# Performance work log

Hardware: AMD Instinct MI355X
Metric: run time of the kernel (lower is better)

Reference implementation:

```python
import jax, jax.numpy as jnp
import numpy as np

LRELU = 0.2


def _gru(x, Wi, Wh, bi, bh):
    # x: [B,T,D]; Wi: [3H,D]; Wh: [3H,H]; PyTorch GRU equations.
    B, T, D = x.shape
    H = Wh.shape[1]
    xW = jnp.einsum('btd,gd->btg', x, Wi) + bi  # precompute input projections
    def step(h, xw):
        gh = h @ Wh.T + bh
        xr, xz, xn = jnp.split(xw, 3, axis=-1)
        hr, hz, hn = jnp.split(gh, 3, axis=-1)
        r = jax.nn.sigmoid(xr + hr)
        z = jax.nn.sigmoid(xz + hz)
        n = jnp.tanh(xn + r * hn)
        h_new = (1.0 - z) * n + z * h
        return h_new, h_new
    h0 = jnp.zeros((B, H), x.dtype)
    hT, hs = jax.lax.scan(step, h0, jnp.swapaxes(xW, 0, 1))
    return jnp.swapaxes(hs, 0, 1), hT


def _gatv2(x, W, b, a, bias):
    # x: [B,N,F]; W: [2F,E]; lin([v_i||v_j]) == x_i@W1 + x_j@W2 + b (avoids materializing concat)
    F = x.shape[-1]
    W1, W2 = W[:F], W[F:]
    g1 = x @ W1            # [B,N,E]
    g2 = x @ W2 + b        # [B,N,E]
    z = jax.nn.leaky_relu(g1[:, :, None, :] + g2[:, None, :, :], LRELU)  # [B,N,N,E]
    e = jnp.einsum('bije,e->bij', z, a) + bias
    att = jax.nn.softmax(e, axis=2)
    return jax.nn.sigmoid(jnp.einsum('bij,bjf->bif', att, x))


def setup_inputs() -> dict:
    B, W, K, H, KS = 16, 256, 64, 150, 7
    key = jax.random.key(0)
    ks = jax.random.split(key, 32)
    def rn(i, sh, scale):
        return jax.random.normal(ks[i], sh, jnp.float32) * scale
    inp = {}
    inp['x'] = jax.random.normal(ks[0], (B, W, K), jnp.float32)
    inp['conv_w'] = rn(1, (K, K, KS), 1.0 / np.sqrt(K * KS))
    inp['conv_b'] = rn(2, (K,), 0.02)
    inp['fW'] = rn(3, (2 * W, 2 * W), 1.0 / np.sqrt(2 * W))
    inp['fb'] = rn(4, (2 * W,), 0.02)
    inp['fa'] = rn(5, (2 * W,), 1.0 / np.sqrt(2 * W))
    inp['fbias'] = rn(6, (K, K), 0.02)
    inp['tW'] = rn(7, (2 * K, 2 * K), 1.0 / np.sqrt(2 * K))
    inp['tb'] = rn(8, (2 * K,), 0.02)
    inp['ta'] = rn(9, (2 * K,), 1.0 / np.sqrt(2 * K))
    inp['tbias'] = rn(10, (W, W), 0.02)
    inp['gWi'] = rn(11, (3 * H, 3 * K), 1.0 / np.sqrt(H))
    inp['gWh'] = rn(12, (3 * H, H), 1.0 / np.sqrt(H))
    inp['gbi'] = rn(13, (3 * H,), 0.02)
    inp['gbh'] = rn(14, (3 * H,), 0.02)
    inp['f0w'] = rn(15, (H, H), 1.0 / np.sqrt(H))
    inp['f0b'] = rn(16, (H,), 0.02)
    inp['f1w'] = rn(17, (H, K), 1.0 / np.sqrt(H))
    inp['f1b'] = rn(18, (K,), 0.02)
    inp['rWi'] = rn(19, (3 * H, H), 1.0 / np.sqrt(H))
    inp['rWh'] = rn(20, (3 * H, H), 1.0 / np.sqrt(H))
    inp['rbi'] = rn(21, (3 * H,), 0.02)
    inp['rbh'] = rn(22, (3 * H,), 0.02)
    inp['rfw'] = rn(23, (H, K), 1.0 / np.sqrt(H))
    inp['rfb'] = rn(24, (K,), 0.02)
    return inp


def reference(x, conv_w, conv_b, fW, fb, fa, fbias, tW, tb, ta, tbias,
              gWi, gWh, gbi, gbh, f0w, f0b, f1w, f1b,
              rWi, rWh, rbi, rbh, rfw, rfb):
    B, Wsz, K = x.shape
    pad = (conv_w.shape[2] - 1) // 2
    # ConvLayer: permute -> constant pad -> conv1d -> relu -> permute back
    x_ncw = jnp.swapaxes(x, 1, 2)  # [B,K,W]
    x_pad = jnp.pad(x_ncw, ((0, 0), (0, 0), (pad, pad)))
    xc = jax.lax.conv_general_dilated(x_pad, conv_w, (1,), 'VALID',
                                      dimension_numbers=('NCW', 'OIW', 'NCW'))
    xc = jax.nn.relu(xc + conv_b[None, :, None])
    xc = jnp.swapaxes(xc, 1, 2)  # [B,W,K]
    # Feature GAT over nodes (K), temporal GAT over time (W)
    h_feat = jnp.swapaxes(_gatv2(jnp.swapaxes(xc, 1, 2), fW, fb, fa, fbias), 1, 2)  # [B,W,K]
    h_temp = _gatv2(xc, tW, tb, ta, tbias)  # [B,W,K]
    h_cat = jnp.concatenate([xc, h_feat, h_temp], axis=2)  # [B,W,3K]
    _, h_end = _gru(h_cat, gWi, gWh, gbi, gbh)  # [B,H]
    # Forecasting MLP (n_layers=1 -> two Linear layers)
    predictions = jax.nn.relu(h_end @ f0w + f0b) @ f1w + f1b  # [B,K]
    # Reconstruction: repeat_interleave over dim 1 then view(B, W, -1)
    H = h_end.shape[1]
    h_rep = jnp.repeat(h_end, Wsz, axis=1).reshape(B, Wsz, H)
    dec_out, _ = _gru(h_rep, rWi, rWh, rbi, rbh)  # [B,W,H]
    recons = dec_out @ rfw + rfb  # [B,W,K]
    return predictions, recons
```

## Files before the change

kernel.cpp:

```cpp
#include <hip/hip_runtime.h>
#include <hip/hip_fp16.h>

typedef _Float16 h2f __attribute__((ext_vector_type(2)));

__device__ __forceinline__ float dot2f(unsigned a, unsigned b, float c) {
#if __has_builtin(__builtin_amdgcn_fdot2)
  return __builtin_amdgcn_fdot2(__builtin_bit_cast(h2f, a),
                                __builtin_bit_cast(h2f, b), c, false);
#else
  h2f x = __builtin_bit_cast(h2f, a);
  h2f y = __builtin_bit_cast(h2f, b);
  return c + (float)x[0] * (float)y[0] + (float)x[1] * (float)y[1];
#endif
}

__device__ __forceinline__ float sigf(float x) { return 1.0f / (1.0f + __expf(-x)); }
__device__ __forceinline__ float tanhfast(float x) {
  float e = __expf(-2.0f * fabsf(x));
  float r = (1.0f - e) / (1.0f + e);
  return (x < 0.0f) ? -r : r;
}
__device__ __forceinline__ float lrelu(float x) { return x > 0.0f ? x : 0.2f * x; }

__global__ void k_prep(const float* __restrict__ conv_w, const float* __restrict__ gWi,
                       const float* __restrict__ gWh, const float* __restrict__ rWh,
                       const float* __restrict__ rWi,
                       float* __restrict__ cwT, float* __restrict__ gWiT,
                       unsigned* __restrict__ gWhP, unsigned* __restrict__ rWhP,
                       float* __restrict__ pref) {
  const int N0 = 64 * 64 * 7;
  const int N1 = 192 * 450;
  const int N2 = 36000;
  const int N3 = 36000;
  const int N4 = 450;
  int total = N0 + N1 + N2 + N3 + N4;
  for (int idx = blockIdx.x * blockDim.x + threadIdx.x; idx < total;
       idx += gridDim.x * blockDim.x) {
    if (idx < N0) {
      int k = idx & 63; int is = idx >> 6; int i = is / 7; int s = is - i * 7;
      cwT[idx] = conv_w[(k * 64 + i) * 7 + s];
    } else if (idx < N0 + N1) {
      int j = idx - N0; int g = j % 450; int d = j / 450;
      gWiT[j] = gWi[g * 192 + d];
    } else if (idx < N0 + N1 + N2 + N3) {
      int u = idx - (N0 + N1);
      const float* W = gWh;
      unsigned* dst = gWhP;
      if (u >= N2) { u -= N2; W = rWh; dst = rWhP; }
      int c = u & 3; int q = u >> 2;
      int i = q / 600; int t6 = q - i * 600;
      int i2 = t6 >> 2, qt = t6 & 3;
      int gg = i / 5, li = i - gg * 5;
      int jj = qt * 20 + li * 4 + c;
      int e0 = 2 * jj, e1 = 2 * jj + 1;
      int row = i2 + gg * 150;
      float a = (e0 < 150) ? W[row * 150 + e0] : 0.f;
      float b = (e1 < 150) ? W[row * 150 + e1] : 0.f;
      __half2 h = __floats2half2_rn(a, b);
      dst[u] = *reinterpret_cast<unsigned*>(&h);
    } else {
      int g = idx - (N0 + N1 + N2 + N3);
      float run = 0.f;
      pref[g] = 0.f;
      for (int j = 0; j < 150; ++j) { run += rWi[g * 150 + j]; pref[(j + 1) * 450 + g] = run; }
    }
  }
}

__global__ __launch_bounds__(256) void k_conv(const float* __restrict__ x,
                                              const float* __restrict__ cwT,
                                              const float* __restrict__ conv_b,
                                              float* __restrict__ xc) {
  __shared__ float xs[22 * 64];
  int b = blockIdx.y, t0 = blockIdx.x * 16, tid = threadIdx.x;
  for (int l = tid; l < 22 * 64; l += 256) {
    int r = l >> 6, i = l & 63;
    int t = t0 - 3 + r;
    xs[l] = (t >= 0 && t < 256) ? x[(b * 256 + t) * 64 + i] : 0.f;
  }
  __syncthreads();
  int k = tid & 63, tg = tid >> 6;
  float bias = conv_b[k];
  float acc[4] = {bias, bias, bias, bias};
  for (int i = 0; i < 64; ++i) {
#pragma unroll
    for (int s = 0; s < 7; ++s) {
      float wv = cwT[(i * 7 + s) * 64 + k];
#pragma unroll
      for (int q = 0; q < 4; ++q)
        acc[q] += xs[(tg * 4 + q + s) * 64 + i] * wv;
    }
  }
#pragma unroll
  for (int q = 0; q < 4; ++q)
    xc[(b * 256 + t0 + tg * 4 + q) * 64 + k] = fmaxf(acc[q], 0.f);
}

__global__ __launch_bounds__(512) void k_featg(const float* __restrict__ xc,
                                               const float* __restrict__ fW,
                                               const float* __restrict__ fb,
                                               float* __restrict__ g1f,
                                               float* __restrict__ g2fT) {
  __shared__ float xsL[256 * 8];
  int b = blockIdx.y, i0 = blockIdx.x * 8, e = threadIdx.x;
  for (int l = e; l < 2048; l += 512) {
    int t = l >> 3, ii = l & 7;
    xsL[l] = xc[(b * 256 + t) * 64 + i0 + ii];
  }
  __syncthreads();
  float a1[8] = {}, a2[8] = {};
  for (int t = 0; t < 256; ++t) {
    float w1 = fW[t * 512 + e];
    float w2 = fW[(256 + t) * 512 + e];
#pragma unroll
    for (int ii = 0; ii < 8; ++ii) {
      float s = xsL[t * 8 + ii];
      a1[ii] += s * w1; a2[ii] += s * w2;
    }
  }
  float fbe = fb[e];
#pragma unroll
  for (int ii = 0; ii < 8; ++ii)
    g1f[(b * 64 + i0 + ii) * 512 + e] = a1[ii];
  float4 v0 = make_float4(a2[0] + fbe, a2[1] + fbe, a2[2] + fbe, a2[3] + fbe);
  float4 v1 = make_float4(a2[4] + fbe, a2[5] + fbe, a2[6] + fbe, a2[7] + fbe);
  float4* p = reinterpret_cast<float4*>(&g2fT[(b * 512 + e) * 64 + i0]);
  p[0] = v0; p[1] = v1;
}

__global__ __launch_bounds__(256) void k_feata(const float* __restrict__ xc,
                                               const float* __restrict__ g1f,
                                               const float* __restrict__ g2fT,
                                               const float* __restrict__ fa,
                                               const float* __restrict__ fbias,
                                               float* __restrict__ h_feat) {
  __shared__ float g1L[512], faL[512], part[4 * 64], attL[64];
  int b = blockIdx.y, i = blockIdx.x, tid = threadIdx.x;
  for (int l = tid; l < 512; l += 256) {
    g1L[l] = g1f[(b * 64 + i) * 512 + l];
    faL[l] = fa[l];
  }
  __syncthreads();
  int q = tid >> 6, j = tid & 63;
  float acc = 0.f;
  for (int e = q * 128; e < q * 128 + 128; ++e) {
    float z = g1L[e] + g2fT[(b * 512 + e) * 64 + j];
    acc += faL[e] * lrelu(z);
  }
  part[q * 64 + j] = acc;
  __syncthreads();
  if (tid < 64) {
    float ev = part[tid] + part[64 + tid] + part[128 + tid] + part[192 + tid] +
               fbias[i * 64 + tid];
    float m = ev;
#pragma unroll
    for (int off = 32; off > 0; off >>= 1) m = fmaxf(m, __shfl_xor(m, off));
    float p = __expf(ev - m);
    float s = p;
#pragma unroll
    for (int off = 32; off > 0; off >>= 1) s += __shfl_xor(s, off);
    attL[tid] = p / s;
  }
  __syncthreads();
  float o = 0.f;
  for (int jj = 0; jj < 64; ++jj)
    o += attL[jj] * xc[(b * 256 + tid) * 64 + jj];
  h_feat[(b * 256 + tid) * 64 + i] = sigf(o);
}

__global__ __launch_bounds__(256) void k_tempg(const float* __restrict__ xc,
                                               const float* __restrict__ tW,
                                               const float* __restrict__ tb,
                                               float* __restrict__ g1t,
                                               float* __restrict__ g2tT) {
  __shared__ float xsL[16 * 64];
  int b = blockIdx.y, t0 = blockIdx.x * 16, tid = threadIdx.x;
  int e = tid & 127, th = tid >> 7;
  for (int l = tid; l < 1024; l += 256)
    xsL[l] = xc[(b * 256 + t0) * 64 + l];
  __syncthreads();
  float a1[8] = {}, a2[8] = {};
  for (int k = 0; k < 64; ++k) {
    float w1 = tW[k * 128 + e];
    float w2 = tW[(64 + k) * 128 + e];
#pragma unroll
    for (int tt = 0; tt < 8; ++tt) {
      float s = xsL[(th * 8 + tt) * 64 + k];
      a1[tt] += s * w1; a2[tt] += s * w2;
    }
  }
  float tbe = tb[e];
#pragma unroll
  for (int tt = 0; tt < 8; ++tt)
    g1t[(b * 256 + t0 + th * 8 + tt) * 128 + e] = a1[tt];
  float4 v0 = make_float4(a2[0] + tbe, a2[1] + tbe, a2[2] + tbe, a2[3] + tbe);
  float4 v1 = make_float4(a2[4] + tbe, a2[5] + tbe, a2[6] + tbe, a2[7] + tbe);
  float4* p = reinterpret_cast<float4*>(&g2tT[(b * 128 + e) * 256 + t0 + th * 8]);
  p[0] = v0; p[1] = v1;
}

__global__ __launch_bounds__(256) void k_tempa(const float* __restrict__ xc,
                                               const float* __restrict__ g1t,
                                               const float* __restrict__ g2tT,
                                               const float* __restrict__ ta,
                                               const float* __restrict__ tbias,
                                               float* __restrict__ h_temp) {
  __shared__ float g1L[4 * 128], taL[128], eL[4 * 256];
  int b = blockIdx.y, i0 = blockIdx.x * 4, tid = threadIdx.x;
  for (int l = tid; l < 512; l += 256)
    g1L[l] = g1t[(b * 256 + i0) * 128 + l];
  if (tid < 128) taL[tid] = ta[tid];
  __syncthreads();
  float acc[4] = {};
  for (int e = 0; e < 128; ++e) {
    float g2 = g2tT[(b * 128 + e) * 256 + tid];
    float tae = taL[e];
#pragma unroll
    for (int ii = 0; ii < 4; ++ii)
      acc[ii] += tae * lrelu(g1L[ii * 128 + e] + g2);
  }
#pragma unroll
  for (int ii = 0; ii < 4; ++ii)
    eL[ii * 256 + tid] = acc[ii] + tbias[(i0 + ii) * 256 + tid];
  __syncthreads();
  int wv = tid >> 6, ln = tid & 63;
  {
    float v0 = eL[wv * 256 + ln], v1 = eL[wv * 256 + 64 + ln];
    float v2 = eL[wv * 256 + 128 + ln], v3 = eL[wv * 256 + 192 + ln];
    float m = fmaxf(fmaxf(v0, v1), fmaxf(v2, v3));
#pragma unroll
    for (int off = 32; off > 0; off >>= 1) m = fmaxf(m, __shfl_xor(m, off));
    float p0 = __expf(v0 - m), p1 = __expf(v1 - m);
    float p2 = __expf(v2 - m), p3 = __expf(v3 - m);
    float s = p0 + p1 + p2 + p3;
#pragma unroll
    for (int off = 32; off > 0; off >>= 1) s += __shfl_xor(s, off);
    float rs = 1.f / s;
    eL[wv * 256 + ln] = p0 * rs; eL[wv * 256 + 64 + ln] = p1 * rs;
    eL[wv * 256 + 128 + ln] = p2 * rs; eL[wv * 256 + 192 + ln] = p3 * rs;
  }
  __syncthreads();
  int ii = tid >> 6, k = tid & 63;
  float o = 0.f;
  for (int j = 0; j < 256; ++j)
    o += eL[ii * 256 + j] * xc[(b * 256 + j) * 64 + k];
  h_temp[(b * 256 + i0 + ii) * 64 + k] = sigf(o);
}

__global__ __launch_bounds__(256) void k_xw(const float* __restrict__ xc,
                                            const float* __restrict__ h_feat,
                                            const float* __restrict__ h_temp,
                                            const float* __restrict__ gWiT,
                                            const float* __restrict__ gbi,
                                            float* __restrict__ xW) {
  __shared__ float hc[16 * 192];
  int b = blockIdx.z, t0 = blockIdx.y * 16, g0 = blockIdx.x * 128;
  int tid = threadIdx.x;
  for (int l = tid; l < 16 * 192; l += 256) {
    int tt = l / 192, d = l - tt * 192;
    int row = (b * 256 + t0 + tt) * 64;
    float v;
    if (d < 64) v = xc[row + d];
    else if (d < 128) v = h_feat[row + d - 64];
    else v = h_temp[row + d - 128];
    hc[l] = v;
  }
  __syncthreads();
  int gl = tid & 127, th = tid >> 7;
  int g = g0 + gl;
  if (g < 450) {
    float acc[8] = {};
    for (int d = 0; d < 192; ++d) {
      float w = gWiT[d * 450 + g];
#pragma unroll
      for (int tt = 0; tt < 8; ++tt)
        acc[tt] += hc[(th * 8 + tt) * 192 + d] * w;
    }
    float bi = gbi[g];
#pragma unroll
    for (int tt = 0; tt < 8; ++tt)
      xW[(b * 256 + t0 + th * 8 + tt) * 450 + g] = acc[tt] + bi;
  }
}

#define D4(HH, WW, A, A2)            \
  A  = dot2f(HH.x, WW.x, A);         \
  A2 = dot2f(HH.y, WW.y, A2);        \
  A  = dot2f(HH.z, WW.z, A);         \
  A2 = dot2f(HH.w, WW.w, A2);

template <int MODE>
__global__ __launch_bounds__(640, 2) void k_gru(const float* __restrict__ xwAll,
                                                const uint4* __restrict__ WhP4,
                                                const float* __restrict__ bh,
                                                const float* __restrict__ pref,
                                                const float* __restrict__ rbi,
                                                const float* __restrict__ h_end_in,
                                                float* __restrict__ h_end,
                                                float* __restrict__ dec_out) {
  __shared__ __align__(16) uint4 hbuf[2][20];
  __shared__ float heL[152];
  int b = blockIdx.x, tid = threadIdx.x;
  bool act = tid < 600;
  int t6 = act ? tid : (tid - 600);
  int i2 = t6 >> 2, qt = t6 & 3;
  {
    unsigned* hz = reinterpret_cast<unsigned*>(&hbuf[0][0]);
    if (tid < 160) hz[tid] = 0u;
  }

  const uint4* Wp = WhP4 + t6;
  uint4 wr0 = Wp[0],         wr1 = Wp[600],      wr2 = Wp[2 * 600],
        wr3 = Wp[3 * 600],   wr4 = Wp[4 * 600];
  uint4 wz0 = Wp[5 * 600],   wz1 = Wp[6 * 600],  wz2 = Wp[7 * 600],
        wz3 = Wp[8 * 600],   wz4 = Wp[9 * 600];
  uint4 wn0 = Wp[10 * 600],  wn1 = Wp[11 * 600], wn2 = Wp[12 * 600],
        wn3 = Wp[13 * 600],  wn4 = Wp[14 * 600];

  float bhr = bh[i2], bhz = bh[i2 + 150], bhn = bh[i2 + 300];
  float bir = 0.f, biz = 0.f, bin_ = 0.f, totr = 0.f, totz = 0.f, totn = 0.f;
  if (MODE == 1) {
    if (tid < 152) heL[tid] = (tid < 150) ? h_end_in[b * 150 + tid] : 0.f;
    bir = rbi[i2]; biz = rbi[i2 + 150]; bin_ = rbi[i2 + 300];
    totr = pref[150 * 450 + i2];
    totz = pref[150 * 450 + i2 + 150];
    totn = pref[150 * 450 + i2 + 300];
  }
  const float* xwrow = xwAll ? (xwAll + (size_t)b * 256 * 450) : nullptr;

  auto ld3 = [&](int t, float& d0, float& d1, float& d2) {
    if (MODE == 0) {
      const float* p = xwrow + t * 450 + i2;
      d0 = p[0]; d1 = p[150]; d2 = p[300];
    } else {
      int base = 150 * t; int a = base >> 8;
      int c = 256 * (a + 1) - base; if (c > 150) c = 150;
      const float* p = pref + c * 450 + i2;
      d0 = p[0]; d1 = p[150]; d2 = p[300];
    }
  };

  float p0a, p0b, p0c;
  ld3(0, p0a, p0b, p0c);
  __syncthreads();

  float hprev = 0.f;
  __half* hout_base = reinterpret_cast<__half*>(&hbuf[0][0]);
#pragma unroll 2
  for (int t = 0; t < 256; ++t) {
    float q0 = 0.f, q1 = 0.f, q2 = 0.f;
    if (t + 1 < 256) ld3(t + 1, q0, q1, q2);

    const uint4* hq = &hbuf[t & 1][qt * 5];
    uint4 h0 = hq[0], h1 = hq[1], h2 = hq[2], h3 = hq[3], h4 = hq[4];
    float ar = 0.f, ar2 = 0.f, az = 0.f, az2 = 0.f, an = 0.f, an2 = 0.f;
    D4(h0, wr0, ar, ar2) D4(h1, wr1, ar, ar2) D4(h2, wr2, ar, ar2)
    D4(h3, wr3, ar, ar2) D4(h4, wr4, ar, ar2)
    D4(h0, wz0, az, az2) D4(h1, wz1, az, az2) D4(h2, wz2, az, az2)
    D4(h3, wz3, az, az2) D4(h4, wz4, az, az2)
    D4(h0, wn0, an, an2) D4(h1, wn1, an, an2) D4(h2, wn2, an, an2)
    D4(h3, wn3, an, an2) D4(h4, wn4, an, an2)
    ar += ar2; az += az2; an += an2;
    ar += __shfl_xor(ar, 1); ar += __shfl_xor(ar, 2);
    az += __shfl_xor(az, 1); az += __shfl_xor(az, 2);
    an += __shfl_xor(an, 1); an += __shfl_xor(an, 2);
    ar += bhr; az += bhz; an += bhn;

    float xr, xz, xn;
    if (MODE == 0) {
      xr = p0a; xz = p0b; xn = p0c;
    } else {
      int base = 150 * t; int a = base >> 8;
      float hA = heL[a], hB = heL[a + 1];
      xr = bir + hA * p0a + hB * (totr - p0a);
      xz = biz + hA * p0b + hB * (totz - p0b);
      xn = bin_ + hA * p0c + hB * (totn - p0c);
    }
    float r = sigf(xr + ar);
    float z = sigf(xz + az);
    float n = tanhfast(xn + r * an);
    float hn = (1.f - z) * n + z * hprev;
    hprev = hn;
    if (act && qt == 0) {
      hout_base[((t & 1) ^ 1) * 160 + i2] = __float2half(hn);
      if (MODE == 1) dec_out[((size_t)(b * 256) + t) * 150 + i2] = hn;
    }
    p0a = q0; p0b = q1; p0c = q2;
    __syncthreads();
  }
  if (MODE == 0 && act && qt == 0) h_end[b * 150 + i2] = hprev;
}

__global__ __launch_bounds__(192) void k_pred(const float* __restrict__ h_end,
                                              const float* __restrict__ f0w,
                                              const float* __restrict__ f0b,
                                              const float* __restrict__ f1w,
                                              const float* __restrict__ f1b,
                                              float* __restrict__ out) {
  __shared__ float heL[152], t1L[152];
  int b = blockIdx.x, tid = threadIdx.x;
  if (tid < 152) heL[tid] = (tid < 150) ? h_end[b * 150 + tid] : 0.f;
  __syncthreads();
  if (tid < 150) {
    float a = f0b[tid];
    for (int i = 0; i < 150; ++i) a += heL[i] * f0w[i * 150 + tid];
    t1L[tid] = fmaxf(a, 0.f);
  }
  if (tid >= 150 && tid < 152) t1L[tid] = 0.f;
  __syncthreads();
  if (tid < 64) {
    float a = f1b[tid];
    for (int j = 0; j < 150; ++j) a += t1L[j] * f1w[j * 64 + tid];
    out[b * 64 + tid] = a;
  }
}

__global__ __launch_bounds__(256) void k_recon(const float* __restrict__ dec_out,
                                               const float* __restrict__ rfw,
                                               const float* __restrict__ rfb,
                                               float* __restrict__ out) {
  int row = blockIdx.x * 4 + (threadIdx.x >> 6);
  int k = threadIdx.x & 63;
  const float* d = dec_out + (size_t)row * 150;
  float a = rfb[k];
  for (int j = 0; j < 150; ++j) a += d[j] * rfw[j * 64 + k];
  out[1024 + (size_t)row * 64 + k] = a;
}

extern "C" void kernel_launch(void* const* d_in, const int* in_sizes, int n_in,
                              void* d_out, int out_size, void* d_ws, size_t ws_size,
                              hipStream_t stream) {
  (void)in_sizes; (void)n_in; (void)out_size; (void)ws_size;
  const float* x      = (const float*)d_in[0];
  const float* conv_w = (const float*)d_in[1];
  const float* conv_b = (const float*)d_in[2];
  const float* fW     = (const float*)d_in[3];
  const float* fb     = (const float*)d_in[4];
  const float* fa     = (const float*)d_in[5];
  const float* fbias  = (const float*)d_in[6];
  const float* tW     = (const float*)d_in[7];
  const float* tb     = (const float*)d_in[8];
  const float* ta     = (const float*)d_in[9];
  const float* tbias  = (const float*)d_in[10];
  const float* gWi    = (const float*)d_in[11];
  const float* gWh    = (const float*)d_in[12];
  const float* gbi    = (const float*)d_in[13];
  const float* gbh    = (const float*)d_in[14];
  const float* f0w    = (const float*)d_in[15];
  const float* f0b    = (const float*)d_in[16];
  const float* f1w    = (const float*)d_in[17];
  const float* f1b    = (const float*)d_in[18];
  const float* rWi    = (const float*)d_in[19];
  const float* rWh    = (const float*)d_in[20];
  const float* rbi    = (const float*)d_in[21];
  const float* rbh    = (const float*)d_in[22];
  const float* rfw    = (const float*)d_in[23];
  const float* rfb    = (const float*)d_in[24];
  float* out = (float*)d_out;
  float* ws  = (float*)d_ws;

  float* XC   = ws;
  float* HF   = XC + 262144;
  float* HT   = HF + 262144;
  float* GBUF = HT + 262144;
  float* G1F  = GBUF;
  float* G2FT = GBUF + 524288;
  float* G1T  = GBUF + 1048576;
  float* G2TT = GBUF + 1572864;
  float* XW   = GBUF;
  float* HEND = GBUF + 2097152;
  float* DEC  = HEND + 2400;
  float* CWT  = DEC + 614400;
  float* GWIT = CWT + 28672;
  unsigned* GWHP = (unsigned*)(GWIT + 86400);
  unsigned* RWHP = GWHP + 36000;
  float* PREF = (float*)(RWHP + 36000);

  k_prep<<<512, 256, 0, stream>>>(conv_w, gWi, gWh, rWh, rWi, CWT, GWIT, GWHP, RWHP, PREF);
  k_conv<<<dim3(16, 16), 256, 0, stream>>>(x, CWT, conv_b, XC);
  k_featg<<<dim3(8, 16), 512, 0, stream>>>(XC, fW, fb, G1F, G2FT);
  k_tempg<<<dim3(16, 16), 256, 0, stream>>>(XC, tW, tb, G1T, G2TT);
  k_feata<<<dim3(64, 16), 256, 0, stream>>>(XC, G1F, G2FT, fa, fbias, HF);
  k_tempa<<<dim3(64, 16), 256, 0, stream>>>(XC, G1T, G2TT, ta, tbias, HT);
  k_xw<<<dim3(4, 16, 16), 256, 0, stream>>>(XC, HF, HT, GWIT, gbi, XW);
  k_gru<0><<<16, 640, 0, stream>>>(XW, (const uint4*)GWHP, gbh, nullptr, nullptr, nullptr, HEND, nullptr);
  k_pred<<<16, 192, 0, stream>>>(HEND, f0w, f0b, f1w, f1b, out);
  k_gru<1><<<16, 640, 0, stream>>>(nullptr, (const uint4*)RWHP, rbh, PREF, rbi, HEND, nullptr, DEC);
  k_recon<<<1024, 256, 0, stream>>>(DEC, rfw, rfb, out);
}
```

Measured before the change: 734.3 us.

## Split GRU recurrent weights across LDS and per-step global loads, use DPP reductions

The recurrent weights were held entirely in registers (15 uint4 per thread). Now six of them are staged in shared memory and the other nine are reloaded from global memory (L1/L2) on every timestep. This cuts register pressure, and the launch-bounds occupancy hint of 2 blocks is dropped. The quad reductions switch from __shfl_xor to DPP quad_perm adds, which avoids ds_bpermute traffic. The cost is extra LDS and global load traffic on the serial critical path of each step.

```diff
diff --git a/kernel.cpp b/kernel.cpp
--- a/kernel.cpp
+++ b/kernel.cpp
@@ -12,6 +12,12 @@
   h2f y = __builtin_bit_cast(h2f, b);
   return c + (float)x[0] * (float)y[0] + (float)x[1] * (float)y[1];
 #endif
+}
+
+template <int CTRL>
+__device__ __forceinline__ float qxor_add(float v) {
+  int r = __builtin_amdgcn_update_dpp(0, __builtin_bit_cast(int, v), CTRL, 0xF, 0xF, true);
+  return v + __builtin_bit_cast(float, r);
 }
 
 __device__ __forceinline__ float sigf(float x) { return 1.0f / (1.0f + __expf(-x)); }
@@ -290,14 +296,15 @@
   A2 = dot2f(HH.w, WW.w, A2);
 
 template <int MODE>
-__global__ __launch_bounds__(640, 2) void k_gru(const float* __restrict__ xwAll,
-                                                const uint4* __restrict__ WhP4,
-                                                const float* __restrict__ bh,
-                                                const float* __restrict__ pref,
-                                                const float* __restrict__ rbi,
-                                                const float* __restrict__ h_end_in,
-                                                float* __restrict__ h_end,
-                                                float* __restrict__ dec_out) {
+__global__ __launch_bounds__(640) void k_gru(const float* __restrict__ xwAll,
+                                             const uint4* __restrict__ WhP4,
+                                             const float* __restrict__ bh,
+                                             const float* __restrict__ pref,
+                                             const float* __restrict__ rbi,
+                                             const float* __restrict__ h_end_in,
+                                             float* __restrict__ h_end,
+                                             float* __restrict__ dec_out) {
+  __shared__ __align__(16) uint4 wlds[600 * 6];
   __shared__ __align__(16) uint4 hbuf[2][20];
   __shared__ float heL[152];
   int b = blockIdx.x, tid = threadIdx.x;
@@ -310,12 +317,10 @@
   }
 
   const uint4* Wp = WhP4 + t6;
-  uint4 wr0 = Wp[0],         wr1 = Wp[600],      wr2 = Wp[2 * 600],
-        wr3 = Wp[3 * 600],   wr4 = Wp[4 * 600];
-  uint4 wz0 = Wp[5 * 600],   wz1 = Wp[6 * 600],  wz2 = Wp[7 * 600],
-        wz3 = Wp[8 * 600],   wz4 = Wp[9 * 600];
-  uint4 wn0 = Wp[10 * 600],  wn1 = Wp[11 * 600], wn2 = Wp[12 * 600],
-        wn3 = Wp[13 * 600],  wn4 = Wp[14 * 600];
+  if (act) {
+#pragma unroll
+    for (int i = 0; i < 6; ++i) wlds[t6 * 6 + i] = Wp[i * 600];
+  }
 
   float bhr = bh[i2], bhz = bh[i2 + 150], bhn = bh[i2 + 300];
   float bir = 0.f, biz = 0.f, bin_ = 0.f, totr = 0.f, totz = 0.f, totn = 0.f;
@@ -348,22 +353,32 @@
   __half* hout_base = reinterpret_cast<__half*>(&hbuf[0][0]);
 #pragma unroll 2
   for (int t = 0; t < 256; ++t) {
+    uint4 sz1 = Wp[6 * 600],  sz2 = Wp[7 * 600],  sz3 = Wp[8 * 600],
+          sz4 = Wp[9 * 600];
+    uint4 sn0 = Wp[10 * 600], sn1 = Wp[11 * 600], sn2 = Wp[12 * 600],
+          sn3 = Wp[13 * 600], sn4 = Wp[14 * 600];
+
     float q0 = 0.f, q1 = 0.f, q2 = 0.f;
     if (t + 1 < 256) ld3(t + 1, q0, q1, q2);
 
+    const uint4* wl = &wlds[t6 * 6];
+    uint4 lr0 = wl[0], lr1 = wl[1], lr2 = wl[2], lr3 = wl[3], lr4 = wl[4];
+    uint4 lz0 = wl[5];
+
     const uint4* hq = &hbuf[t & 1][qt * 5];
     uint4 h0 = hq[0], h1 = hq[1], h2 = hq[2], h3 = hq[3], h4 = hq[4];
+
     float ar = 0.f, ar2 = 0.f, az = 0.f, az2 = 0.f, an = 0.f, an2 = 0.f;
-    D4(h0, wr0, ar, ar2) D4(h1, wr1, ar, ar2) D4(h2, wr2, ar, ar2)
-    D4(h3, wr3, ar, ar2) D4(h4, wr4, ar, ar2)
-    D4(h0, wz0, az, az2) D4(h1, wz1, az, az2) D4(h2, wz2, az, az2)
-    D4(h3, wz3, az, az2) D4(h4, wz4, az, az2)
-    D4(h0, wn0, an, an2) D4(h1, wn1, an, an2) D4(h2, wn2, an, an2)
-    D4(h3, wn3, an, an2) D4(h4, wn4, an, an2)
+    D4(h0, lr0, ar, ar2) D4(h1, lr1, ar, ar2) D4(h2, lr2, ar, ar2)
+    D4(h3, lr3, ar, ar2) D4(h4, lr4, ar, ar2)
+    D4(h0, lz0, az, az2) D4(h1, sz1, az, az2) D4(h2, sz2, az, az2)
+    D4(h3, sz3, az, az2) D4(h4, sz4, az, az2)
+    D4(h0, sn0, an, an2) D4(h1, sn1, an, an2) D4(h2, sn2, an, an2)
+    D4(h3, sn3, an, an2) D4(h4, sn4, an, an2)
     ar += ar2; az += az2; an += an2;
-    ar += __shfl_xor(ar, 1); ar += __shfl_xor(ar, 2);
-    az += __shfl_xor(az, 1); az += __shfl_xor(az, 2);
-    an += __shfl_xor(an, 1); an += __shfl_xor(an, 2);
+    ar = qxor_add<0xB1>(ar); ar = qxor_add<0x4E>(ar);
+    az = qxor_add<0xB1>(az); az = qxor_add<0x4E>(az);
+    an = qxor_add<0xB1>(an); an = qxor_add<0x4E>(an);
     ar += bhr; az += bhz; an += bhn;
 
     float xr, xz, xn;
```

Result: slower. 762.9 us (+3.9%).
